# Optimization experiments

Hardware: AMD Instinct MI355X
Metric: run time of the kernel (lower is better)

Reference implementation:

```python
import jax, jax.numpy as jnp
from jax import lax
import numpy as np

B = 262144   # batch of independent series
K = 64       # forecast horizon (init k)
D_IN = 200   # Non_AR_net input dim (Linear(200,100))
H = 100      # hidden width


def setup_inputs() -> dict:
    key = jax.random.key(0)
    ks = jax.random.split(key, 10)
    f32 = jnp.float32
    x = jax.random.normal(ks[0], (B, D_IN), f32)
    last_mu = jax.random.normal(ks[1], (B,), f32)
    # last_sigma is the variance state; keep it strictly positive
    last_sigma = jax.random.uniform(ks[2], (B,), f32) + 0.5
    # MLP params (Kaiming-ish scale)
    W1 = jax.random.normal(ks[3], (D_IN, H), f32) / np.float32(np.sqrt(D_IN))
    b1 = jnp.zeros((H,), f32)
    W2 = jax.random.normal(ks[4], (H, H), f32) / np.float32(np.sqrt(H))
    b2 = jnp.zeros((H,), f32)
    W3 = jax.random.normal(ks[5], (H, K), f32) / np.float32(np.sqrt(H))
    b3 = jnp.zeros((K,), f32)
    return {
        "x": x, "last_mu": last_mu, "last_sigma": last_sigma,
        "alpha_mu": jnp.asarray(0.1, f32), "alpha_sigma": jnp.asarray(0.1, f32),
        "beta_mu": jnp.asarray(0.9, f32), "beta_sigma": jnp.asarray(0.85, f32),
        "omega_mu": jnp.asarray(0.0, f32), "omega_sigma": jnp.asarray(0.05, f32),
        "nu": jnp.asarray(5.0, f32), "norm_strength": jnp.asarray(1.0, f32),
        "W1": W1, "b1": b1, "W2": W2, "b2": b2, "W3": W3, "b3": b3,
    }


def _mlp(x, W1, b1, W2, b2, W3, b3):
    h = jax.nn.relu(x @ W1 + b1)
    h = jax.nn.relu(h @ W2 + b2)
    return h @ W3 + b3  # [B, K]


def _ar_gas(deep_preds, last_mu, last_sigma, a_mu, a_s, b_mu, b_s, o_mu, o_s, nu, ns):
    """Student-t score-driven (GAS) k-step recurrence, vectorized over batch.
    deep_preds: [B, K]; state mu, sigma2: [B]."""
    w = 1.0 + 1.0 / nu

    def step(carry, y):  # y: [B]
        mu, s2 = carry
        e = y - mu
        denom = 1.0 + e * e / (nu * s2)
        mu_new = o_mu + ns * a_mu * (w * e / denom) + b_mu * mu
        s2_new = o_s + ns * a_s * (w * e * e / denom - s2) + b_s * s2
        return (mu_new, s2_new), (mu_new, s2_new)

    (_, _), (mus, s2s) = lax.scan(step, (last_mu, last_sigma), deep_preds.T)
    return mus.T, jnp.sqrt(s2s.T)  # [B, K] each


def reference(x, last_mu, last_sigma, alpha_mu, alpha_sigma, beta_mu, beta_sigma,
              omega_mu, omega_sigma, nu, norm_strength,
              W1, b1, W2, b2, W3, b3):
    deep_preds = _mlp(x, W1, b1, W2, b2, W3, b3)            # [B, K]
    dp = lax.stop_gradient(deep_preds)                       # .detach() in torch
    mu_pred, sigma_pred = _ar_gas(dp, last_mu, last_sigma,
                                  alpha_mu, alpha_sigma, beta_mu, beta_sigma,
                                  omega_mu, omega_sigma, nu, norm_strength)
    return deep_preds * sigma_pred + mu_pred                 # [B, K]
```

## Files before the change

### kernel.cpp

```cpp
#include <hip/hip_runtime.h>
#include <hip/hip_bf16.h>

typedef short v8s __attribute__((ext_vector_type(8)));
typedef float v4f __attribute__((ext_vector_type(4)));

#define THREADS 512
#define WAVES   8
#define BMROWS  256
#define NFRAGS  96
#define W1F     0
#define W2F     49
#define W3F     77
#define FRAG_BYTES (NFRAGS * 1024)
#define SLAB_BASE  FRAG_BYTES
#define LDS_TOTAL  (FRAG_BYTES + WAVES * 8192)

__device__ __forceinline__ unsigned short f2bf(float f) {
    union { __hip_bfloat16 h; unsigned short u; } c;
    c.h = __float2bfloat16(f);
    return c.u;
}
__device__ __forceinline__ unsigned pk2(float a, float b) {
    return (unsigned)f2bf(a) | ((unsigned)f2bf(b) << 16);
}
__device__ __forceinline__ v4f mfma16(v8s a, v8s b, v4f c) {
    return __builtin_amdgcn_mfma_f32_16x16x32_bf16(a, b, c, 0, 0, 0);
}
__device__ __forceinline__ v8s mkfrag(float4 a, float4 b) {
    union { unsigned u[4]; v8s s; } t;
    t.u[0] = pk2(a.x, a.y); t.u[1] = pk2(a.z, a.w);
    t.u[2] = pk2(b.x, b.y); t.u[3] = pk2(b.z, b.w);
    return t.s;
}
__device__ __forceinline__ void gload_lds16(const void* g, void* l) {
    __builtin_amdgcn_global_load_lds(
        (const __attribute__((address_space(1))) void*)g,
        (__attribute__((address_space(3))) void*)l, 16, 0, 0);
}

__global__ void prep_weights(const float* __restrict__ W1,
                             const float* __restrict__ W2,
                             const float* __restrict__ W3,
                             uint4* __restrict__ wf) {
    const int bid = blockIdx.x, l = threadIdx.x;
    const float* W; int K, N, KC, base, f;
    if (bid < 49)      { W = W1; K = 200; N = 100; KC = 7; base = W1F * 64; f = bid; }
    else if (bid < 77) { W = W2; K = 100; N = 100; KC = 4; base = W2F * 64; f = bid - 49; }
    else               { W = W3; K = 100; N = 64;  KC = 4; base = W3F * 64; f = bid - 77; }
    const int kc = f % KC;
    const int n  = (f / KC) * 16 + (l & 15);
    unsigned u[4];
    #pragma unroll
    for (int p = 0; p < 4; ++p) {
        const int k0 = kc * 32 + (l >> 4) * 8 + p * 2;
        const float a = (k0     < K && n < N) ? W[(size_t)k0 * N + n]       : 0.f;
        const float b = (k0 + 1 < K && n < N) ? W[(size_t)(k0 + 1) * N + n] : 0.f;
        u[p] = pk2(a, b);
    }
    wf[base + f * 64 + l] = make_uint4(u[0], u[1], u[2], u[3]);
}

__device__ __forceinline__ int sladdr(int wid, int row, int byte) {
    return SLAB_BASE + (wid << 13) + (row << 8) +
           ((((byte >> 4) ^ row) & 15) << 4) + (byte & 15);
}

__global__ __launch_bounds__(THREADS, 2)
void ar_gas_v10(const float* __restrict__ x,
                const float* __restrict__ last_mu,
                const float* __restrict__ last_sigma,
                const float* __restrict__ p_amu, const float* __restrict__ p_as,
                const float* __restrict__ p_bmu, const float* __restrict__ p_bs,
                const float* __restrict__ p_omu, const float* __restrict__ p_os,
                const float* __restrict__ p_nu,  const float* __restrict__ p_ns,
                const float* __restrict__ b1, const float* __restrict__ b2,
                const float* __restrict__ b3,
                const uint4* __restrict__ wf,
                float* __restrict__ out)
{
    extern __shared__ __align__(16) unsigned char L[];
    const int tid  = threadIdx.x;
    const int lane = tid & 63;
    const int wid  = tid >> 6;
    const int l15  = lane & 15;
    const int l4   = lane >> 4;
    const int blk  = blockIdx.x;

    {
        const uint4* gsrc = wf + (wid * 12) * 64 + lane;
        unsigned char* ldst = L + (wid * 12) * 1024;
        #pragma unroll
        for (int j = 0; j < 12; ++j)
            gload_lds16(gsrc + j * 64, ldst + j * 1024);
    }
    __syncthreads();

#define FRAG(f) (*(const uint4*)(&L[(f) * 1024 + lane * 16]))

    const size_t gw = (size_t)blk * BMROWS + (size_t)wid * 32;
    const float* xp0 = x + (gw + l15) * 200;
    const float* xp1 = x + (gw + 16 + l15) * 200;

#define XLOAD(d0, d1, xp, kk)                                           \
    { int kb = (kk) * 32 + l4 * 8;                                      \
      kb = (kb + 8 <= 200) ? kb : 168;                                  \
      d0 = *(const float4*)((xp) + kb);                                 \
      d1 = *(const float4*)((xp) + kb + 4); }

    v4f acc[2][7];
    #pragma unroll
    for (int mt = 0; mt < 2; ++mt)
        #pragma unroll
        for (int nt = 0; nt < 7; ++nt) acc[mt][nt] = (v4f){0.f, 0.f, 0.f, 0.f};
    float bv[7];
    #pragma unroll
    for (int nt = 0; nt < 7; ++nt) {
        const int c = nt * 16 + l15;
        bv[nt] = (c < 100) ? b1[c] : 0.f;
    }

    float4 c0a, c0b, c1a, c1b;
    XLOAD(c0a, c0b, xp0, 0);
    XLOAD(c1a, c1b, xp1, 0);
    #pragma unroll
    for (int kc = 0; kc < 7; ++kc) {
        uint4 bu[7];
        #pragma unroll
        for (int nt = 0; nt < 7; ++nt) bu[nt] = FRAG(W1F + nt * 7 + kc);
        const v8s af0 = mkfrag(c0a, c0b);
        const v8s af1 = mkfrag(c1a, c1b);
        if (kc < 6) {
            XLOAD(c0a, c0b, xp0, kc + 1);
            XLOAD(c1a, c1b, xp1, kc + 1);
        }
        #pragma unroll
        for (int nt = 0; nt < 7; ++nt) {
            const v8s bf = *(const v8s*)&bu[nt];
            acc[0][nt] = mfma16(af0, bf, acc[0][nt]);
            acc[1][nt] = mfma16(af1, bf, acc[1][nt]);
        }
    }
#undef XLOAD

    #pragma unroll
    for (int mt = 0; mt < 2; ++mt)
        #pragma unroll
        for (int nt = 0; nt < 7; ++nt) {
            #pragma unroll
            for (int r = 0; r < 4; ++r) {
                const int row = mt * 16 + l4 * 4 + r;
                const int c   = nt * 16 + l15;
                const float v = fmaxf(acc[mt][nt][r] + bv[nt], 0.f);
                *(unsigned short*)(&L[sladdr(wid, row, c * 2)]) = f2bf(v);
            }
        }
    *(uint4*)(&L[sladdr(wid, lane >> 1, 224 + (lane & 1) * 16)]) =
        make_uint4(0, 0, 0, 0);

    v4f acc2[2][7];
    #pragma unroll
    for (int mt = 0; mt < 2; ++mt)
        #pragma unroll
        for (int nt = 0; nt < 7; ++nt) acc2[mt][nt] = (v4f){0.f, 0.f, 0.f, 0.f};
    float bv2[7];
    #pragma unroll
    for (int nt = 0; nt < 7; ++nt) {
        const int c = nt * 16 + l15;
        bv2[nt] = (c < 100) ? b2[c] : 0.f;
    }
    #pragma unroll
    for (int kc = 0; kc < 4; ++kc) {
        uint4 bu[7];
        #pragma unroll
        for (int nt = 0; nt < 7; ++nt) bu[nt] = FRAG(W2F + nt * 4 + kc);
        uint4 t0 = *(const uint4*)(&L[sladdr(wid, l15,      kc * 64 + l4 * 16)]);
        uint4 t1 = *(const uint4*)(&L[sladdr(wid, 16 + l15, kc * 64 + l4 * 16)]);
        const v8s af0 = *(v8s*)&t0;
        const v8s af1 = *(v8s*)&t1;
        #pragma unroll
        for (int nt = 0; nt < 7; ++nt) {
            const v8s bf = *(const v8s*)&bu[nt];
            acc2[0][nt] = mfma16(af0, bf, acc2[0][nt]);
            acc2[1][nt] = mfma16(af1, bf, acc2[1][nt]);
        }
    }
    #pragma unroll
    for (int mt = 0; mt < 2; ++mt)
        #pragma unroll
        for (int nt = 0; nt < 7; ++nt) {
            #pragma unroll
            for (int r = 0; r < 4; ++r) {
                const int row = mt * 16 + l4 * 4 + r;
                const int c   = nt * 16 + l15;
                const float v = fmaxf(acc2[mt][nt][r] + bv2[nt], 0.f);
                *(unsigned short*)(&L[sladdr(wid, row, c * 2)]) = f2bf(v);
            }
        }

    v4f acc3[2][4];
    #pragma unroll
    for (int mt = 0; mt < 2; ++mt)
        #pragma unroll
        for (int nt = 0; nt < 4; ++nt) acc3[mt][nt] = (v4f){0.f, 0.f, 0.f, 0.f};
    float bv3[4];
    #pragma unroll
    for (int nt = 0; nt < 4; ++nt) bv3[nt] = b3[nt * 16 + l15];

    #pragma unroll
    for (int kc = 0; kc < 4; ++kc) {
        uint4 bu[4];
        #pragma unroll
        for (int nt = 0; nt < 4; ++nt) bu[nt] = FRAG(W3F + nt * 4 + kc);
        uint4 t0 = *(const uint4*)(&L[sladdr(wid, l15,      kc * 64 + l4 * 16)]);
        uint4 t1 = *(const uint4*)(&L[sladdr(wid, 16 + l15, kc * 64 + l4 * 16)]);
        const v8s af0 = *(v8s*)&t0;
        const v8s af1 = *(v8s*)&t1;
        #pragma unroll
        for (int nt = 0; nt < 4; ++nt) {
            const v8s bf = *(const v8s*)&bu[nt];
            acc3[0][nt] = mfma16(af0, bf, acc3[0][nt]);
            acc3[1][nt] = mfma16(af1, bf, acc3[1][nt]);
        }
    }
#undef FRAG
    #pragma unroll
    for (int mt = 0; mt < 2; ++mt)
        #pragma unroll
        for (int nt = 0; nt < 4; ++nt) {
            #pragma unroll
            for (int r = 0; r < 4; ++r) {
                const int row = mt * 16 + l4 * 4 + r;
                const int c   = nt * 16 + l15;
                *(float*)(&L[sladdr(wid, row, c * 4)]) = acc3[mt][nt][r] + bv3[nt];
            }
        }

    if (lane < 32) {
        const size_t rg = gw + lane;
        float mu = last_mu[rg];
        float s2 = last_sigma[rg];
        const float anu = *p_nu,  ans = *p_ns;
        const float aMu = *p_amu, aSg = *p_as;
        const float bMu = *p_bmu, bSg = *p_bs;
        const float oMu = *p_omu, oSg = *p_os;
        const float w   = 1.f + __builtin_amdgcn_rcpf(anu);
        const float cmu = ans * aMu * w;
        const float cs  = ans * aSg * w;
        const float bs2 = bSg - ans * aSg;

#define GAS_STEP(Y, O)                                                  \
        {   const float e    = (Y) - mu;                                \
            const float nus2 = anu * s2;                                \
            const float den  = fmaf(e, e, nus2);                        \
            const float r0   = __builtin_amdgcn_rcpf(den);              \
            const float p    = e * nus2 * r0;                           \
            mu = fmaf(cmu, p, fmaf(bMu, mu, oMu));                      \
            s2 = fmaf(cs, e * p, fmaf(bs2, s2, oSg));                   \
            (O) = fmaf((Y), __builtin_amdgcn_sqrtf(s2), mu); }

        #pragma unroll
        for (int q = 0; q < 16; ++q) {
            float4 d = *(float4*)(&L[sladdr(wid, lane, q * 16)]);
            float o0, o1, o2, o3;
            GAS_STEP(d.x, o0); GAS_STEP(d.y, o1);
            GAS_STEP(d.z, o2); GAS_STEP(d.w, o3);
            *(float4*)(&L[sladdr(wid, lane, q * 16)]) = make_float4(o0, o1, o2, o3);
        }
#undef GAS_STEP
    }

    #pragma unroll
    for (int i = 0; i < 8; ++i) {
        const int fi  = i * 64 + lane;
        const int row = fi >> 4, q = fi & 15;
        float4 v = *(float4*)(&L[sladdr(wid, row, q * 16)]);
        ((float4*)out)[gw * 16 + fi] = v;
    }
}

extern "C" void kernel_launch(void* const* d_in, const int* in_sizes, int n_in,
                              void* d_out, int out_size, void* d_ws, size_t ws_size,
                              hipStream_t stream) {
    const float* x          = (const float*)d_in[0];
    const float* last_mu    = (const float*)d_in[1];
    const float* last_sigma = (const float*)d_in[2];
    const float* amu        = (const float*)d_in[3];
    const float* asig       = (const float*)d_in[4];
    const float* bmu        = (const float*)d_in[5];
    const float* bsig       = (const float*)d_in[6];
    const float* omu        = (const float*)d_in[7];
    const float* osig       = (const float*)d_in[8];
    const float* nu         = (const float*)d_in[9];
    const float* ns         = (const float*)d_in[10];
    const float* W1         = (const float*)d_in[11];
    const float* b1         = (const float*)d_in[12];
    const float* W2         = (const float*)d_in[13];
    const float* b2         = (const float*)d_in[14];
    const float* W3         = (const float*)d_in[15];
    const float* b3         = (const float*)d_in[16];
    float* out = (float*)d_out;

    uint4* wf = (uint4*)d_ws;
    prep_weights<<<96, 64, 0, stream>>>(W1, W2, W3, wf);

    hipFuncSetAttribute((const void*)ar_gas_v10,
                        hipFuncAttributeMaxDynamicSharedMemorySize, LDS_TOTAL);

    const int B = in_sizes[1];
    dim3 grid(B / BMROWS), block(THREADS);
    ar_gas_v10<<<grid, block, LDS_TOTAL, stream>>>(
        x, last_mu, last_sigma,
        amu, asig, bmu, bsig, omu, osig, nu, ns,
        b1, b2, b3, wf, out);
}
```

Measured before the change: 91.61 us.

## Shrink blocks and reuse LDS slots across layers to cut shared memory

Halves the block to 4 waves and 128 rows, and overlays weight fragments in LDS. W2 and W1 are loaded first, W1's region is then reused as activation slabs, and W3 fragments are loaded into W2's slots after layer 2. This lowers LDS per block from about 160KB to about 77KB so more blocks can be resident per CU. The cost is extra __syncthreads barriers, a mid-kernel weight reload, and each block reloading weights for fewer rows. It also moves the mu/sigma state loads and the first x loads ahead of the weight staging to hide their latency.

New measurement: 92.42 us. No clear change (+0.9%).

```diff
diff --git a/kernel.cpp b/kernel.cpp
--- a/kernel.cpp
+++ b/kernel.cpp
@@ -4,16 +4,14 @@
 typedef short v8s __attribute__((ext_vector_type(8)));
 typedef float v4f __attribute__((ext_vector_type(4)));
 
-#define THREADS 512
-#define WAVES   8
-#define BMROWS  256
-#define NFRAGS  96
+#define THREADS 256
+#define BMROWS  128
 #define W1F     0
 #define W2F     49
 #define W3F     77
-#define FRAG_BYTES (NFRAGS * 1024)
-#define SLAB_BASE  FRAG_BYTES
-#define LDS_TOTAL  (FRAG_BYTES + WAVES * 8192)
+#define W1LDS   28
+#define SLABB   28672
+#define LDS_TOTAL 78848
 
 __device__ __forceinline__ unsigned short f2bf(float f) {
     union { __hip_bfloat16 h; unsigned short u; } c;
@@ -61,12 +59,12 @@
 }
 
 __device__ __forceinline__ int sladdr(int wid, int row, int byte) {
-    return SLAB_BASE + (wid << 13) + (row << 8) +
+    return SLABB + (wid << 13) + (row << 8) +
            ((((byte >> 4) ^ row) & 15) << 4) + (byte & 15);
 }
 
 __global__ __launch_bounds__(THREADS, 2)
-void ar_gas_v10(const float* __restrict__ x,
+void ar_gas_v12(const float* __restrict__ x,
                 const float* __restrict__ last_mu,
                 const float* __restrict__ last_sigma,
                 const float* __restrict__ p_amu, const float* __restrict__ p_as,
@@ -86,20 +84,12 @@
     const int l4   = lane >> 4;
     const int blk  = blockIdx.x;
 
-    {
-        const uint4* gsrc = wf + (wid * 12) * 64 + lane;
-        unsigned char* ldst = L + (wid * 12) * 1024;
-        #pragma unroll
-        for (int j = 0; j < 12; ++j)
-            gload_lds16(gsrc + j * 64, ldst + j * 1024);
-    }
-    __syncthreads();
-
-#define FRAG(f) (*(const uint4*)(&L[(f) * 1024 + lane * 16]))
-
     const size_t gw = (size_t)blk * BMROWS + (size_t)wid * 32;
     const float* xp0 = x + (gw + l15) * 200;
     const float* xp1 = x + (gw + 16 + l15) * 200;
+
+    const float mu_init = last_mu[gw + (lane & 31)];
+    const float s2_init = last_sigma[gw + (lane & 31)];
 
 #define XLOAD(d0, d1, xp, kk)                                           \
     { int kb = (kk) * 32 + l4 * 8;                                      \
@@ -107,11 +97,10 @@
       d0 = *(const float4*)((xp) + kb);                                 \
       d1 = *(const float4*)((xp) + kb + 4); }
 
-    v4f acc[2][7];
-    #pragma unroll
-    for (int mt = 0; mt < 2; ++mt)
-        #pragma unroll
-        for (int nt = 0; nt < 7; ++nt) acc[mt][nt] = (v4f){0.f, 0.f, 0.f, 0.f};
+    float4 c0a, c0b, c1a, c1b;
+    XLOAD(c0a, c0b, xp0, 0);
+    XLOAD(c1a, c1b, xp1, 0);
+
     float bv[7];
     #pragma unroll
     for (int nt = 0; nt < 7; ++nt) {
@@ -119,14 +108,25 @@
         bv[nt] = (c < 100) ? b1[c] : 0.f;
     }
 
-    float4 c0a, c0b, c1a, c1b;
-    XLOAD(c0a, c0b, xp0, 0);
-    XLOAD(c1a, c1b, xp1, 0);
+    for (int s = wid; s < 77; s += 4) {
+        const int src = (s < 28) ? (W2F + s) : (W1F + s - 28);
+        gload_lds16(wf + src * 64 + lane, L + s * 1024);
+    }
+    __syncthreads();
+
+#define FRAG(slot) (*(const uint4*)(&L[(slot) * 1024 + lane * 16]))
+
+    v4f acc[2][7];
+    #pragma unroll
+    for (int mt = 0; mt < 2; ++mt)
+        #pragma unroll
+        for (int nt = 0; nt < 7; ++nt) acc[mt][nt] = (v4f){0.f, 0.f, 0.f, 0.f};
+
     #pragma unroll
     for (int kc = 0; kc < 7; ++kc) {
         uint4 bu[7];
         #pragma unroll
-        for (int nt = 0; nt < 7; ++nt) bu[nt] = FRAG(W1F + nt * 7 + kc);
+        for (int nt = 0; nt < 7; ++nt) bu[nt] = FRAG(W1LDS + nt * 7 + kc);
         const v8s af0 = mkfrag(c0a, c0b);
         const v8s af1 = mkfrag(c1a, c1b);
         if (kc < 6) {
@@ -141,6 +141,8 @@
         }
     }
 #undef XLOAD
+
+    __syncthreads();
 
     #pragma unroll
     for (int mt = 0; mt < 2; ++mt)
@@ -157,22 +159,23 @@
     *(uint4*)(&L[sladdr(wid, lane >> 1, 224 + (lane & 1) * 16)]) =
         make_uint4(0, 0, 0, 0);
 
-    v4f acc2[2][7];
-    #pragma unroll
-    for (int mt = 0; mt < 2; ++mt)
-        #pragma unroll
-        for (int nt = 0; nt < 7; ++nt) acc2[mt][nt] = (v4f){0.f, 0.f, 0.f, 0.f};
     float bv2[7];
     #pragma unroll
     for (int nt = 0; nt < 7; ++nt) {
         const int c = nt * 16 + l15;
         bv2[nt] = (c < 100) ? b2[c] : 0.f;
     }
+    v4f acc2[2][7];
+    #pragma unroll
+    for (int mt = 0; mt < 2; ++mt)
+        #pragma unroll
+        for (int nt = 0; nt < 7; ++nt) acc2[mt][nt] = (v4f){0.f, 0.f, 0.f, 0.f};
+
     #pragma unroll
     for (int kc = 0; kc < 4; ++kc) {
         uint4 bu[7];
         #pragma unroll
-        for (int nt = 0; nt < 7; ++nt) bu[nt] = FRAG(W2F + nt * 4 + kc);
+        for (int nt = 0; nt < 7; ++nt) bu[nt] = FRAG(nt * 4 + kc);
         uint4 t0 = *(const uint4*)(&L[sladdr(wid, l15,      kc * 64 + l4 * 16)]);
         uint4 t1 = *(const uint4*)(&L[sladdr(wid, 16 + l15, kc * 64 + l4 * 16)]);
         const v8s af0 = *(v8s*)&t0;
@@ -184,6 +187,12 @@
             acc2[1][nt] = mfma16(af1, bf, acc2[1][nt]);
         }
     }
+
+    __syncthreads();
+
+    for (int s = wid; s < 16; s += 4)
+        gload_lds16(wf + (W3F + s) * 64 + lane, L + s * 1024);
+
     #pragma unroll
     for (int mt = 0; mt < 2; ++mt)
         #pragma unroll
@@ -197,20 +206,22 @@
             }
         }
 
+    __syncthreads();
+
+    float bv3[4];
+    #pragma unroll
+    for (int nt = 0; nt < 4; ++nt) bv3[nt] = b3[nt * 16 + l15];
     v4f acc3[2][4];
     #pragma unroll
     for (int mt = 0; mt < 2; ++mt)
         #pragma unroll
         for (int nt = 0; nt < 4; ++nt) acc3[mt][nt] = (v4f){0.f, 0.f, 0.f, 0.f};
-    float bv3[4];
-    #pragma unroll
-    for (int nt = 0; nt < 4; ++nt) bv3[nt] = b3[nt * 16 + l15];
 
     #pragma unroll
     for (int kc = 0; kc < 4; ++kc) {
         uint4 bu[4];
         #pragma unroll
-        for (int nt = 0; nt < 4; ++nt) bu[nt] = FRAG(W3F + nt * 4 + kc);
+        for (int nt = 0; nt < 4; ++nt) bu[nt] = FRAG(nt * 4 + kc);
         uint4 t0 = *(const uint4*)(&L[sladdr(wid, l15,      kc * 64 + l4 * 16)]);
         uint4 t1 = *(const uint4*)(&L[sladdr(wid, 16 + l15, kc * 64 + l4 * 16)]);
         const v8s af0 = *(v8s*)&t0;
@@ -223,6 +234,7 @@
         }
     }
 #undef FRAG
+
     #pragma unroll
     for (int mt = 0; mt < 2; ++mt)
         #pragma unroll
@@ -236,9 +248,8 @@
         }
 
     if (lane < 32) {
-        const size_t rg = gw + lane;
-        float mu = last_mu[rg];
-        float s2 = last_sigma[rg];
+        float mu = mu_init;
+        float s2 = s2_init;
         const float anu = *p_nu,  ans = *p_ns;
         const float aMu = *p_amu, aSg = *p_as;
         const float bMu = *p_bmu, bSg = *p_bs;
@@ -301,14 +312,14 @@
     float* out = (float*)d_out;
 
     uint4* wf = (uint4*)d_ws;
-    prep_weights<<<96, 64, 0, stream>>>(W1, W2, W3, wf);
-
-    hipFuncSetAttribute((const void*)ar_gas_v10,
+    prep_weights<<<93, 64, 0, stream>>>(W1, W2, W3, wf);
+
+    hipFuncSetAttribute((const void*)ar_gas_v12,
                         hipFuncAttributeMaxDynamicSharedMemorySize, LDS_TOTAL);
 
     const int B = in_sizes[1];
     dim3 grid(B / BMROWS), block(THREADS);
-    ar_gas_v10<<<grid, block, LDS_TOTAL, stream>>>(
+    ar_gas_v12<<<grid, block, LDS_TOTAL, stream>>>(
         x, last_mu, last_sigma,
         amu, asig, bmu, bsig, omu, osig, nu, ns,
         b1, b2, b3, wf, out);
```
